# Performance work log

Hardware: AMD Instinct MI355X
Metric: run time of the kernel (lower is better)

The kernel has to match this reference:

```python
import jax, jax.numpy as jnp
import numpy as np

DIM = 256
NUM_HEADS = 8
HEAD_DIM = DIM // NUM_HEADS


def setup_inputs() -> dict:
    key = jax.random.key(0)
    k1, k2, k3, k4 = jax.random.split(key, 4)
    b, n = 4, 2048
    x = jax.random.normal(k1, (b, n, DIM), dtype=jnp.float32)
    # Linear weights with fan-in scaling (matches nn.Linear init magnitude,
    # keeps exp(qk) numerically sane since the original has no max-subtraction).
    Wqkv = jax.random.normal(k2, (DIM, 3 * DIM), dtype=jnp.float32) * (DIM ** -0.5)
    Wout = jax.random.normal(k3, (DIM, DIM), dtype=jnp.float32) * (DIM ** -0.5)
    bout = jax.random.normal(k4, (DIM,), dtype=jnp.float32) * 0.01
    return {"x": x, "Wqkv": Wqkv, "Wout": Wout, "bout": bout}


def reference(x, Wqkv, Wout, bout):
    b, n, d = x.shape
    h, hd = NUM_HEADS, HEAD_DIM
    scale = hd ** -0.5
    qkv = x @ Wqkv  # [b, n, 3d]
    q, k, v = jnp.split(qkv, 3, axis=-1)
    # [b, h, n, hd]
    q = q.reshape(b, n, h, hd).transpose(0, 2, 1, 3) * scale
    k = k.reshape(b, n, h, hd).transpose(0, 2, 1, 3)
    v = v.reshape(b, n, h, hd).transpose(0, 2, 1, 3)
    # Original KeOps path: unnormalized exp (no max-subtraction), separate
    # numerator / denominator reductions, eps in denominator.
    scores = jnp.einsum('bhnd,bhmd->bhnm', q, k)  # [b, h, n, n]
    e = jnp.exp(scores)
    denom = jnp.sum(e, axis=-1, keepdims=True)          # [b, h, n, 1]
    numer = jnp.einsum('bhnm,bhmd->bhnd', e, v)         # [b, h, n, hd]
    out = numer / (denom + 1e-6)
    out = out.transpose(0, 2, 1, 3).reshape(b, n, d)
    return out @ Wout + bout
```

## Files before the change

### kernel.cpp

```cpp
#include <hip/hip_runtime.h>

#define DIM 256
#define NHEADS 8
#define HDIM 32

typedef _Float16 half8_t __attribute__((ext_vector_type(8)));
typedef _Float16 half4_t __attribute__((ext_vector_type(4)));
typedef float float4_t __attribute__((ext_vector_type(4)));

__device__ __forceinline__ float fast_exp2(float x) {
#if __has_builtin(__builtin_amdgcn_exp2f)
    return __builtin_amdgcn_exp2f(x);
#else
    return __expf(x * 0.6931471805599453f);
#endif
}

__device__ __forceinline__ void gload_lds16(const void* g, void* l) {
    __builtin_amdgcn_global_load_lds((const __attribute__((address_space(1))) void*)g,
                                     (__attribute__((address_space(3))) void*)l,
                                     16, 0, 0);
}

__global__ __launch_bounds__(256) void prep(const float* __restrict__ x,
                                            const float* __restrict__ Wqkv,
                                            const float* __restrict__ Wout,
                                            _Float16* __restrict__ xh,
                                            _Float16* __restrict__ WqT,
                                            _Float16* __restrict__ WoT) {
    __shared__ float ts[32][33];
    const int bid = blockIdx.x, t = threadIdx.x;
    if (bid < 1024) {
        size_t idx = (size_t)bid * 2048 + (size_t)t * 8;
        float tmp[8];
        *reinterpret_cast<float4*>(tmp)     = *reinterpret_cast<const float4*>(x + idx);
        *reinterpret_cast<float4*>(tmp + 4) = *reinterpret_cast<const float4*>(x + idx + 4);
        half8_t h;
        #pragma unroll
        for (int j = 0; j < 8; ++j) h[j] = (_Float16)tmp[j];
        *reinterpret_cast<half8_t*>(xh + idx) = h;
    } else {
        const float* src; _Float16* dst; int K, N, kb, nb;
        if (bid < 1024 + 192) { int b2 = bid - 1024; src = Wqkv; dst = WqT; K = 256; N = 768; nb = b2 % 24; kb = b2 / 24; }
        else                  { int b3 = bid - 1216; src = Wout; dst = WoT; K = 256; N = 256; nb = b3 % 8;  kb = b3 / 8; }
        const int tx = t & 31, ty = t >> 5;
        #pragma unroll
        for (int i = 0; i < 4; ++i) {
            int k = kb * 32 + ty + i * 8;
            ts[ty + i * 8][tx] = src[(size_t)k * N + nb * 32 + tx];
        }
        __syncthreads();
        #pragma unroll
        for (int i = 0; i < 4; ++i) {
            int nl = ty + i * 8;
            dst[(size_t)(nb * 32 + nl) * K + kb * 32 + tx] = (_Float16)ts[tx][nl];
        }
    }
}

__global__ __launch_bounds__(256) void gemm_qkv(const _Float16* __restrict__ A,
                                                const _Float16* __restrict__ BT,
                                                _Float16* __restrict__ Cv,
                                                _Float16* __restrict__ VTo) {
    constexpr int K = 256, ldc = 512;
    __shared__ alignas(16) _Float16 As[64 * 32];
    __shared__ alignas(16) _Float16 Bs[128 * 32];
    const int t = threadIdx.x, lane = t & 63, wave = t >> 6;
    const int l16 = lane & 15, quad = lane >> 4;
    const int m0 = blockIdx.y * 64, n0 = blockIdx.x * 128;
    const int wr = (wave >> 1) * 32, wc = (wave & 1) * 64;
    constexpr float QS = 0.17677669529663687f * 1.4426950408889634f;
    float4_t acc[2][4];
    #pragma unroll
    for (int i = 0; i < 2; ++i)
        #pragma unroll
        for (int j = 0; j < 4; ++j) acc[i][j] = (float4_t){0.f, 0.f, 0.f, 0.f};

    const int srow = lane >> 2;
    const int scol = (lane & 3) * 8;

    for (int k0 = 0; k0 < K; k0 += 32) {
        {
            int chunk = wave;
            int r = chunk * 16 + srow;
            gload_lds16(A + (size_t)(m0 + r) * K + k0 + scol, As + chunk * 512);
        }
        #pragma unroll
        for (int i = 0; i < 2; ++i) {
            int chunk = i * 4 + wave;
            int r = chunk * 16 + srow;
            gload_lds16(BT + (size_t)(n0 + r) * K + k0 + scol, Bs + chunk * 512);
        }
        __syncthreads();
        half8_t af[2], bf[4];
        #pragma unroll
        for (int i = 0; i < 2; ++i)
            af[i] = *reinterpret_cast<const half8_t*>(As + (wr + i * 16 + l16) * 32 + quad * 8);
        #pragma unroll
        for (int j = 0; j < 4; ++j)
            bf[j] = *reinterpret_cast<const half8_t*>(Bs + (wc + j * 16 + l16) * 32 + quad * 8);
        #pragma unroll
        for (int i = 0; i < 2; ++i)
            #pragma unroll
            for (int j = 0; j < 4; ++j)
                acc[i][j] = __builtin_amdgcn_mfma_f32_16x16x32_f16(af[i], bf[j], acc[i][j], 0, 0, 0);
        __syncthreads();
    }

    if (n0 >= 512) {
        const int bb = m0 >> 11;
        const int tok0 = (m0 & 2047) + wr;
        #pragma unroll
        for (int i = 0; i < 2; ++i)
            #pragma unroll
            for (int j = 0; j < 4; ++j) {
                int vcol = n0 + wc + j * 16 + l16 - 512;
                int hh = vcol >> 5, d = vcol & 31;
                half4_t p;
                #pragma unroll
                for (int r = 0; r < 4; ++r) p[r] = (_Float16)acc[i][j][r];
                *reinterpret_cast<half4_t*>(
                    VTo + ((size_t)(bb * NHEADS + hh) * HDIM + d) * 2048
                        + tok0 + i * 16 + quad * 4) = p;
            }
    } else {
        #pragma unroll
        for (int i = 0; i < 2; ++i)
            #pragma unroll
            for (int r = 0; r < 4; ++r) {
                int row = m0 + wr + i * 16 + quad * 4 + r;
                #pragma unroll
                for (int j = 0; j < 4; ++j) {
                    int col = n0 + wc + j * 16 + l16;
                    float v = acc[i][j][r];
                    if (n0 < 256) v *= QS;
                    Cv[(size_t)row * ldc + col] = (_Float16)v;
                }
            }
    }
}


#define GLD(dst, addr) \
    asm volatile("global_load_dwordx4 %0, %1, off" : "=v"(dst) : "v"(addr))
#define WAITV(N) asm volatile("s_waitcnt vmcnt(" #N ")" ::: "memory")
#define SB0 __builtin_amdgcn_sched_barrier(0)

#define LOADASM(P, k0)                                            \
    do {                                                          \
        const _Float16* kp_ = kbase + (size_t)(k0) * 512;         \
        GLD(k##P[0], kp_);                                        \
        GLD(k##P[1], kp_ + (size_t)16 * 512);                     \
        GLD(k##P[2], kp_ + (size_t)32 * 512);                     \
        GLD(k##P[3], kp_ + (size_t)48 * 512);                     \
        const _Float16* vp_ = vbase + (k0);                       \
        GLD(v##P[0], vp_);                                        \
        GLD(v##P[1], vp_ + (size_t)16 * 2048);                    \
        GLD(v##P[2], vp_ + 32);                                   \
        GLD(v##P[3], vp_ + 32 + (size_t)16 * 2048);               \
    } while (0)

#define STEP(P)                                                                    \
    do {                                                                           \
        half4_t ep[4][4];                                                          \
        _Pragma("unroll")                                                          \
        for (int kb = 0; kb < 4; ++kb)                                             \
            _Pragma("unroll")                                                      \
            for (int g = 0; g < 4; ++g) {                                          \
                float4_t st = __builtin_amdgcn_mfma_f32_16x16x32_f16(              \
                    k##P[kb], qf[g], z, 0, 0, 0);                                  \
                auto lo = __builtin_amdgcn_cvt_pkrtz(fast_exp2(st[0]),             \
                                                     fast_exp2(st[1]));            \
                auto hi = __builtin_amdgcn_cvt_pkrtz(fast_exp2(st[2]),             \
                                                     fast_exp2(st[3]));            \
                ep[kb][g] = (half4_t){(_Float16)lo[0], (_Float16)lo[1],            \
                                      (_Float16)hi[0], (_Float16)hi[1]};           \
            }                                                                      \
        _Pragma("unroll")                                                          \
        for (int s = 0; s < 2; ++s) {                                              \
            _Pragma("unroll")                                                      \
            for (int tt = 0; tt < 2; ++tt)                                         \
                _Pragma("unroll")                                                  \
                for (int g = 0; g < 4; ++g)                                        \
                    *reinterpret_cast<half4_t*>(                                   \
                        esw + (g * 16 + l16) * 40 + tt * 16 + quad * 4) =          \
                        ep[s * 2 + tt][g];                                         \
            _Pragma("unroll")                                                      \
            for (int g = 0; g < 4; ++g) {                                          \
                half8_t ef = *reinterpret_cast<const half8_t*>(                    \
                    esw + (g * 16 + l16) * 40 + quad * 8);                         \
                num[g][0] = __builtin_amdgcn_mfma_f32_16x16x32_f16(                \
                    ef, v##P[s * 2], num[g][0], 0, 0, 0);                          \
                num[g][1] = __builtin_amdgcn_mfma_f32_16x16x32_f16(                \
                    ef, v##P[s * 2 + 1], num[g][1], 0, 0, 0);                      \
                dacc[g] = __builtin_amdgcn_mfma_f32_16x16x32_f16(                  \
                    ef, onef, dacc[g], 0, 0, 0);                                   \
            }                                                                      \
        }                                                                          \
    } while (0)

__global__ __launch_bounds__(256, 2) void attn_v11(const _Float16* __restrict__ qkh,
                                                   const _Float16* __restrict__ VT,
                                                   _Float16* __restrict__ NUM,
                                                   float* __restrict__ DEN) {
    __shared__ alignas(16) _Float16 es[4][64][40];
    const int bid = ((blockIdx.x & 7) << 6) | (blockIdx.x >> 3);
    const int kh = bid & 1;
    const int qb = (bid >> 1) & 7;
    const int bh = bid >> 4;
    const int b = bh >> 3, h = bh & 7;
    const int t = threadIdx.x, lane = t & 63, wave = t >> 6;
    const int l16 = lane & 15, quad = lane >> 4;
    const int bN = b * 2048;
    const int q0w = qb * 256 + wave * 64;
    const int kbeg = kh * 1024;

    const _Float16* kbase = qkh + (size_t)(bN + l16) * 512 + 256 + h * HDIM + quad * 8;
    const _Float16* vbase = VT + (size_t)bh * HDIM * 2048 + (size_t)l16 * 2048 + quad * 8;

    float4_t num[4][2];
    #pragma unroll
    for (int g = 0; g < 4; ++g)
        #pragma unroll
        for (int dt = 0; dt < 2; ++dt) num[g][dt] = (float4_t){0.f, 0.f, 0.f, 0.f};
    float4_t dacc[4];
    #pragma unroll
    for (int g = 0; g < 4; ++g) dacc[g] = (float4_t){0.f, 0.f, 0.f, 0.f};

    half8_t onef;
    #pragma unroll
    for (int j = 0; j < 8; ++j) onef[j] = (_Float16)1.0f;

    _Float16* esw = &es[wave][0][0];
    const float4_t z = {0.f, 0.f, 0.f, 0.f};

    half8_t qf[4];
    {
        const _Float16* qrow = qkh + (size_t)(bN + q0w + l16) * 512 + h * HDIM + quad * 8;
        GLD(qf[0], qrow);
        GLD(qf[1], qrow + (size_t)16 * 512);
        GLD(qf[2], qrow + (size_t)32 * 512);
        GLD(qf[3], qrow + (size_t)48 * 512);
    }

    half8_t kA[4], vA[4], kB[4], vB[4];
    LOADASM(A, kbeg);
    for (int k0 = kbeg; k0 < kbeg + 1024; k0 += 128) {
        LOADASM(B, k0 + 64);
        WAITV(8);
        SB0;
        __builtin_amdgcn_s_setprio(1);
        STEP(A);
        __builtin_amdgcn_s_setprio(0);
        if (k0 + 128 < kbeg + 1024) {
            LOADASM(A, k0 + 128);
            WAITV(8);
        } else {
            WAITV(0);
        }
        SB0;
        __builtin_amdgcn_s_setprio(1);
        STEP(B);
        __builtin_amdgcn_s_setprio(0);
    }

    _Float16* ob = NUM + (size_t)kh * 2097152 + (size_t)(bN + q0w) * DIM + h * HDIM;
    #pragma unroll
    for (int g = 0; g < 4; ++g)
        #pragma unroll
        for (int r = 0; r < 4; ++r) {
            size_t ro = (size_t)(g * 16 + quad * 4 + r) * DIM;
            ob[ro + l16]      = (_Float16)num[g][0][r];
            ob[ro + 16 + l16] = (_Float16)num[g][1][r];
        }
    if (l16 == 0) {
        #pragma unroll
        for (int g = 0; g < 4; ++g)
            #pragma unroll
            for (int r = 0; r < 4; ++r)
                DEN[kh * 65536 + bh * 2048 + q0w + g * 16 + quad * 4 + r] = dacc[g][r];
    }
}

__global__ __launch_bounds__(256) void gemm_out(const _Float16* __restrict__ NUM,
                                                const float* __restrict__ DEN,
                                                const _Float16* __restrict__ BT,
                                                const float* __restrict__ bias,
                                                float* __restrict__ C) {
    constexpr int K = 256;
    __shared__ alignas(16) _Float16 As[64 * 32];
    __shared__ alignas(16) _Float16 Bs[128 * 32];
    const int t = threadIdx.x, lane = t & 63, wave = t >> 6;
    const int l16 = lane & 15, quad = lane >> 4;
    const int m0 = blockIdx.y * 64, n0 = blockIdx.x * 128;
    const int wr = (wave >> 1) * 32, wc = (wave & 1) * 64;
    float4_t acc[2][4];
    #pragma unroll
    for (int i = 0; i < 2; ++i)
        #pragma unroll
        for (int j = 0; j < 4; ++j) acc[i][j] = (float4_t){0.f, 0.f, 0.f, 0.f};

    const int srow = lane >> 2;
    const int scol = (lane & 3) * 8;
    const int ar = t >> 2;
    const int ac = (t & 3) * 8;
    const int row = m0 + ar;
    const int bb = row >> 11, tok = row & 2047;

    for (int k0 = 0; k0 < K; k0 += 32) {
        {
            const int h = k0 >> 5;
            const int di = (bb * 8 + h) * 2048 + tok;
            float den = DEN[di] + DEN[di + 65536] + 1e-6f;
            _Float16 rcp = (_Float16)(1.0f / den);
            size_t idx = (size_t)row * 256 + k0 + ac;
            half8_t nu0 = *reinterpret_cast<const half8_t*>(NUM + idx);
            half8_t nu1 = *reinterpret_cast<const half8_t*>(NUM + idx + 2097152);
            *reinterpret_cast<half8_t*>(As + ar * 32 + ac) = (nu0 + nu1) * rcp;
        }
        #pragma unroll
        for (int i = 0; i < 2; ++i) {
            int chunk = i * 4 + wave;
            int r = chunk * 16 + srow;
            gload_lds16(BT + (size_t)(n0 + r) * K + k0 + scol, Bs + chunk * 512);
        }
        __syncthreads();
        half8_t af[2], bf[4];
        #pragma unroll
        for (int i = 0; i < 2; ++i)
            af[i] = *reinterpret_cast<const half8_t*>(As + (wr + i * 16 + l16) * 32 + quad * 8);
        #pragma unroll
        for (int j = 0; j < 4; ++j)
            bf[j] = *reinterpret_cast<const half8_t*>(Bs + (wc + j * 16 + l16) * 32 + quad * 8);
        #pragma unroll
        for (int i = 0; i < 2; ++i)
            #pragma unroll
            for (int j = 0; j < 4; ++j)
                acc[i][j] = __builtin_amdgcn_mfma_f32_16x16x32_f16(af[i], bf[j], acc[i][j], 0, 0, 0);
        __syncthreads();
    }

    float bv[4];
    #pragma unroll
    for (int j = 0; j < 4; ++j) bv[j] = bias[n0 + wc + j * 16 + l16];
    #pragma unroll
    for (int i = 0; i < 2; ++i)
        #pragma unroll
        for (int r = 0; r < 4; ++r) {
            int orow = m0 + wr + i * 16 + quad * 4 + r;
            #pragma unroll
            for (int j = 0; j < 4; ++j) {
                int col = n0 + wc + j * 16 + l16;
                C[(size_t)orow * DIM + col] = acc[i][j][r] + bv[j];
            }
        }
}

extern "C" void kernel_launch(void* const* d_in, const int* in_sizes, int n_in,
                              void* d_out, int out_size, void* d_ws, size_t ws_size,
                              hipStream_t stream) {
    const float* x    = (const float*)d_in[0];
    const float* Wqkv = (const float*)d_in[1];
    const float* Wout = (const float*)d_in[2];
    const float* bout = (const float*)d_in[3];
    float* out = (float*)d_out;
    const int M = 8192;

    _Float16* xh    = (_Float16*)d_ws;
    _Float16* WqT   = xh + (size_t)M * DIM;
    _Float16* WoT   = WqT + 768 * 256;
    _Float16* qkh   = WoT + 256 * 256;
    _Float16* vt    = qkh + (size_t)M * 512;
    _Float16* NUM   = vt + (size_t)32 * HDIM * 2048;
    float*    DEN   = (float*)(NUM + (size_t)2 * M * DIM);

    hipLaunchKernelGGL(prep, dim3(1280), dim3(256), 0, stream, x, Wqkv, Wout, xh, WqT, WoT);
    hipLaunchKernelGGL(gemm_qkv, dim3(6, 128), dim3(256), 0, stream, xh, WqT, qkh, vt);
    hipLaunchKernelGGL(attn_v11, dim3(512), dim3(256), 0, stream, qkh, vt, NUM, DEN);
    hipLaunchKernelGGL(gemm_out, dim3(2, 128), dim3(256), 0, stream,
                       NUM, DEN, WoT, bout, out);
}
```

Before: 121.4 us.

## Stage K/V tiles cooperatively in swizzled LDS with double buffering

Previously each of the four waves in a block loaded the same K and V chunks from global memory straight into registers. The kernel now has the block load each 64-key K/V chunk once into double-buffered LDS with async global-to-LDS loads, and waves read their fragments from there. XOR swizzles on the K, V and exp-score LDS layouts are meant to avoid bank conflicts. This cuts redundant global/L2 traffic, but adds LDS reads and a block-wide barrier every chunk, and drops the hand-scheduled register prefetch pipeline.

```diff
diff --git a/kernel.cpp b/kernel.cpp
--- a/kernel.cpp
+++ b/kernel.cpp
@@ -141,68 +141,65 @@
 }
 
 
-#define GLD(dst, addr) \
-    asm volatile("global_load_dwordx4 %0, %1, off" : "=v"(dst) : "v"(addr))
-#define WAITV(N) asm volatile("s_waitcnt vmcnt(" #N ")" ::: "memory")
-#define SB0 __builtin_amdgcn_sched_barrier(0)
-
-#define LOADASM(P, k0)                                            \
-    do {                                                          \
-        const _Float16* kp_ = kbase + (size_t)(k0) * 512;         \
-        GLD(k##P[0], kp_);                                        \
-        GLD(k##P[1], kp_ + (size_t)16 * 512);                     \
-        GLD(k##P[2], kp_ + (size_t)32 * 512);                     \
-        GLD(k##P[3], kp_ + (size_t)48 * 512);                     \
-        const _Float16* vp_ = vbase + (k0);                       \
-        GLD(v##P[0], vp_);                                        \
-        GLD(v##P[1], vp_ + (size_t)16 * 2048);                    \
-        GLD(v##P[2], vp_ + 32);                                   \
-        GLD(v##P[3], vp_ + 32 + (size_t)16 * 2048);               \
+#define STAGE(bf_, ch_)                                                        \
+    do {                                                                       \
+        gload_lds16(ksrc + (size_t)(ch_) * 32768, &Ks[bf_][0][0] + wave * 512);\
+        gload_lds16(vsrc + (ch_) * 64,            &Vs[bf_][0][0] + wave * 512);\
     } while (0)
 
-#define STEP(P)                                                                    \
-    do {                                                                           \
-        half4_t ep[4][4];                                                          \
-        _Pragma("unroll")                                                          \
-        for (int kb = 0; kb < 4; ++kb)                                             \
-            _Pragma("unroll")                                                      \
-            for (int g = 0; g < 4; ++g) {                                          \
-                float4_t st = __builtin_amdgcn_mfma_f32_16x16x32_f16(              \
-                    k##P[kb], qf[g], z, 0, 0, 0);                                  \
-                auto lo = __builtin_amdgcn_cvt_pkrtz(fast_exp2(st[0]),             \
-                                                     fast_exp2(st[1]));            \
-                auto hi = __builtin_amdgcn_cvt_pkrtz(fast_exp2(st[2]),             \
-                                                     fast_exp2(st[3]));            \
-                ep[kb][g] = (half4_t){(_Float16)lo[0], (_Float16)lo[1],            \
-                                      (_Float16)hi[0], (_Float16)hi[1]};           \
-            }                                                                      \
-        _Pragma("unroll")                                                          \
-        for (int s = 0; s < 2; ++s) {                                              \
-            _Pragma("unroll")                                                      \
-            for (int tt = 0; tt < 2; ++tt)                                         \
-                _Pragma("unroll")                                                  \
-                for (int g = 0; g < 4; ++g)                                        \
-                    *reinterpret_cast<half4_t*>(                                   \
-                        esw + (g * 16 + l16) * 40 + tt * 16 + quad * 4) =          \
-                        ep[s * 2 + tt][g];                                         \
-            _Pragma("unroll")                                                      \
-            for (int g = 0; g < 4; ++g) {                                          \
-                half8_t ef = *reinterpret_cast<const half8_t*>(                    \
-                    esw + (g * 16 + l16) * 40 + quad * 8);                         \
-                num[g][0] = __builtin_amdgcn_mfma_f32_16x16x32_f16(                \
-                    ef, v##P[s * 2], num[g][0], 0, 0, 0);                          \
-                num[g][1] = __builtin_amdgcn_mfma_f32_16x16x32_f16(                \
-                    ef, v##P[s * 2 + 1], num[g][1], 0, 0, 0);                      \
-                dacc[g] = __builtin_amdgcn_mfma_f32_16x16x32_f16(                  \
-                    ef, onef, dacc[g], 0, 0, 0);                                   \
-            }                                                                      \
-        }                                                                          \
+#define COMPUTE(bf_)                                                           \
+    do {                                                                       \
+        half4_t ep[4][4];                                                      \
+        _Pragma("unroll")                                                      \
+        for (int kb = 0; kb < 4; ++kb) {                                       \
+            half8_t kf = *reinterpret_cast<const half8_t*>(                    \
+                &Ks[bf_][kb * 16 + l16][kswz * 8]);                            \
+            _Pragma("unroll")                                                  \
+            for (int g = 0; g < 4; ++g) {                                      \
+                float4_t st = __builtin_amdgcn_mfma_f32_16x16x32_f16(          \
+                    kf, qf[g], z, 0, 0, 0);                                    \
+                auto lo = __builtin_amdgcn_cvt_pkrtz(fast_exp2(st[0]),         \
+                                                     fast_exp2(st[1]));        \
+                auto hi = __builtin_amdgcn_cvt_pkrtz(fast_exp2(st[2]),         \
+                                                     fast_exp2(st[3]));        \
+                ep[kb][g] = (half4_t){(_Float16)lo[0], (_Float16)lo[1],        \
+                                      (_Float16)hi[0], (_Float16)hi[1]};       \
+            }                                                                  \
+        }                                                                      \
+        _Pragma("unroll")                                                      \
+        for (int s = 0; s < 2; ++s) {                                          \
+            _Pragma("unroll")                                                  \
+            for (int tt = 0; tt < 2; ++tt)                                     \
+                _Pragma("unroll")                                              \
+                for (int g = 0; g < 4; ++g)                                    \
+                    *reinterpret_cast<half4_t*>(                               \
+                        esw + (g * 16 + l16) * 40 +                            \
+                        ((tt * 2 + (quad >> 1)) ^ esz) * 8 + (quad & 1) * 4) = \
+                        ep[s * 2 + tt][g];                                     \
+            half8_t vf0 = *reinterpret_cast<const half8_t*>(                   \
+                &Vs[bf_][l16][((s * 4 + quad) ^ vsz) * 8]);                    \
+            half8_t vf1 = *reinterpret_cast<const half8_t*>(                   \
+                &Vs[bf_][16 + l16][((s * 4 + quad) ^ vsz) * 8]);               \
+            _Pragma("unroll")                                                  \
+            for (int g = 0; g < 4; ++g) {                                      \
+                half8_t ef = *reinterpret_cast<const half8_t*>(                \
+                    esw + (g * 16 + l16) * 40 + (quad ^ esz) * 8);             \
+                num[g][0] = __builtin_amdgcn_mfma_f32_16x16x32_f16(            \
+                    ef, vf0, num[g][0], 0, 0, 0);                              \
+                num[g][1] = __builtin_amdgcn_mfma_f32_16x16x32_f16(            \
+                    ef, vf1, num[g][1], 0, 0, 0);                              \
+                dacc[g] = __builtin_amdgcn_mfma_f32_16x16x32_f16(              \
+                    ef, onef, dacc[g], 0, 0, 0);                               \
+            }                                                                  \
+        }                                                                      \
     } while (0)
 
-__global__ __launch_bounds__(256, 2) void attn_v11(const _Float16* __restrict__ qkh,
+__global__ __launch_bounds__(256, 2) void attn_v12(const _Float16* __restrict__ qkh,
                                                    const _Float16* __restrict__ VT,
                                                    _Float16* __restrict__ NUM,
                                                    float* __restrict__ DEN) {
+    __shared__ alignas(16) _Float16 Ks[2][64][32];
+    __shared__ alignas(16) _Float16 Vs[2][32][64];
     __shared__ alignas(16) _Float16 es[4][64][40];
     const int bid = ((blockIdx.x & 7) << 6) | (blockIdx.x >> 3);
     const int kh = bid & 1;
@@ -215,53 +212,51 @@
     const int q0w = qb * 256 + wave * 64;
     const int kbeg = kh * 1024;
 
-    const _Float16* kbase = qkh + (size_t)(bN + l16) * 512 + 256 + h * HDIM + quad * 8;
-    const _Float16* vbase = VT + (size_t)bh * HDIM * 2048 + (size_t)l16 * 2048 + quad * 8;
-
-    float4_t num[4][2];
-    #pragma unroll
-    for (int g = 0; g < 4; ++g)
-        #pragma unroll
-        for (int dt = 0; dt < 2; ++dt) num[g][dt] = (float4_t){0.f, 0.f, 0.f, 0.f};
-    float4_t dacc[4];
-    #pragma unroll
-    for (int g = 0; g < 4; ++g) dacc[g] = (float4_t){0.f, 0.f, 0.f, 0.f};
-
-    half8_t onef;
-    #pragma unroll
-    for (int j = 0; j < 8; ++j) onef[j] = (_Float16)1.0f;
-
-    _Float16* esw = &es[wave][0][0];
-    const float4_t z = {0.f, 0.f, 0.f, 0.f};
+    const int uk = (lane & 3) ^ ((lane >> 3) & 3);
+    const _Float16* ksrc = qkh + (size_t)(bN + kbeg + wave * 16 + (lane >> 2)) * 512
+                               + 256 + h * HDIM + uk * 8;
+    const int uv = (lane & 7) ^ (lane >> 3);
+    const _Float16* vsrc = VT + (size_t)bh * HDIM * 2048
+                              + (size_t)(wave * 8 + (lane >> 3)) * 2048
+                              + kbeg + uv * 8;
+    const int kswz = quad ^ ((l16 >> 1) & 3);
+    const int vsz = l16 & 7;
+    const int esz = l16 & 3;
 
     half8_t qf[4];
     {
         const _Float16* qrow = qkh + (size_t)(bN + q0w + l16) * 512 + h * HDIM + quad * 8;
-        GLD(qf[0], qrow);
-        GLD(qf[1], qrow + (size_t)16 * 512);
-        GLD(qf[2], qrow + (size_t)32 * 512);
-        GLD(qf[3], qrow + (size_t)48 * 512);
-    }
-
-    half8_t kA[4], vA[4], kB[4], vB[4];
-    LOADASM(A, kbeg);
-    for (int k0 = kbeg; k0 < kbeg + 1024; k0 += 128) {
-        LOADASM(B, k0 + 64);
-        WAITV(8);
-        SB0;
+        #pragma unroll
+        for (int g = 0; g < 4; ++g)
+            qf[g] = *reinterpret_cast<const half8_t*>(qrow + (size_t)g * 16 * 512);
+    }
+
+    float4_t num[4][2];
+    #pragma unroll
+    for (int g = 0; g < 4; ++g)
+        #pragma unroll
+        for (int dt = 0; dt < 2; ++dt) num[g][dt] = (float4_t){0.f, 0.f, 0.f, 0.f};
+    float4_t dacc[4];
+    #pragma unroll
+    for (int g = 0; g < 4; ++g) dacc[g] = (float4_t){0.f, 0.f, 0.f, 0.f};
+
+    half8_t onef;
+    #pragma unroll
+    for (int j = 0; j < 8; ++j) onef[j] = (_Float16)1.0f;
+
+    _Float16* esw = &es[wave][0][0];
+    const float4_t z = {0.f, 0.f, 0.f, 0.f};
+
+    STAGE(0, 0);
+    __syncthreads();
+    int bf = 0;
+    for (int ch = 0; ch < 16; ++ch) {
+        if (ch + 1 < 16) STAGE(bf ^ 1, ch + 1);
         __builtin_amdgcn_s_setprio(1);
-        STEP(A);
+        COMPUTE(bf);
         __builtin_amdgcn_s_setprio(0);
-        if (k0 + 128 < kbeg + 1024) {
-            LOADASM(A, k0 + 128);
-            WAITV(8);
-        } else {
-            WAITV(0);
-        }
-        SB0;
-        __builtin_amdgcn_s_setprio(1);
-        STEP(B);
-        __builtin_amdgcn_s_setprio(0);
+        __syncthreads();
+        bf ^= 1;
     }
 
     _Float16* ob = NUM + (size_t)kh * 2097152 + (size_t)(bN + q0w) * DIM + h * HDIM;
@@ -376,7 +371,7 @@
 
     hipLaunchKernelGGL(prep, dim3(1280), dim3(256), 0, stream, x, Wqkv, Wout, xh, WqT, WoT);
     hipLaunchKernelGGL(gemm_qkv, dim3(6, 128), dim3(256), 0, stream, xh, WqT, qkh, vt);
-    hipLaunchKernelGGL(attn_v11, dim3(512), dim3(256), 0, stream, qkh, vt, NUM, DEN);
+    hipLaunchKernelGGL(attn_v12, dim3(512), dim3(256), 0, stream, qkh, vt, NUM, DEN);
     hipLaunchKernelGGL(gemm_out, dim3(2, 128), dim3(256), 0, stream,
                        NUM, DEN, WoT, bout, out);
 }
```

New measurement: 130.1 us. 1.07x slower.
